# Kernel optimization log

Hardware: AMD Instinct MI355X
Metric: run time of the kernel (lower is better)

## Reference

```python
import jax, jax.numpy as jnp
import numpy as np

N_NODES = 100000
N_EDGES = 1600000
NHID = 128
NFEAT = 256


def setup_inputs() -> dict:
    key = jax.random.key(0)
    ks = jax.random.split(key, 7)
    x = jax.random.normal(ks[0], (N_NODES, NHID), dtype=jnp.float32)
    edge_index = jax.random.randint(ks[1], (2, N_EDGES), 0, N_NODES, dtype=jnp.int64)
    edge_weight = jax.random.uniform(ks[2], (N_EDGES,), dtype=jnp.float32)
    W1 = jax.random.normal(ks[3], (NHID, NHID), dtype=jnp.float32) * (1.0 / np.sqrt(NHID))
    b1 = jnp.zeros((NHID,), dtype=jnp.float32)
    W2 = jax.random.normal(ks[4], (NHID, NFEAT), dtype=jnp.float32) * (1.0 / np.sqrt(NHID))
    b2 = jnp.zeros((NFEAT,), dtype=jnp.float32)
    return {"x": x, "edge_weight": edge_weight, "W1": W1, "b1": b1,
            "W2": W2, "b2": b2, "edge_index": edge_index}


def _gcn_layer(x, W, b, src, dst, w, num_nodes):
    # support = x @ W ; out = spmm(adj, support) + b  (adj given as weighted edge list)
    support = x @ W                                  # [N, d_out]
    msg = support[src] * w[:, None]                  # gather + scale: [E, d_out]
    agg = jax.ops.segment_sum(msg, dst, num_segments=num_nodes)  # scatter-add: [N, d_out]
    return agg + b


def reference(x, edge_weight, W1, b1, W2, b2, edge_index):
    src, dst = edge_index[0], edge_index[1]
    n = x.shape[0]
    # layer 1: GCN -> ReLU (dropout p=0 in eval mode -> identity)
    h = jax.nn.relu(_gcn_layer(x, W1, b1, src, dst, edge_weight, n))
    # layer 2: GCN -> ReLU
    out = jax.nn.relu(_gcn_layer(h, W2, b2, src, dst, edge_weight, n))
    return out
```

## Files before the change

kernel.cpp:

```cpp
#include <hip/hip_runtime.h>
#include <hip/hip_bf16.h>

#define NHID 128
#define NBLK 512
#define FCAP 4096

typedef __attribute__((ext_vector_type(8))) short short8v;
typedef __attribute__((ext_vector_type(4))) float f32x4;

__device__ __forceinline__ unsigned short f32_to_bf16(float f) {
    unsigned u = __float_as_uint(f);
    u += 0x7fffu + ((u >> 16) & 1u);
    return (unsigned short)(u >> 16);
}


__global__ __launch_bounds__(256) void coarse_hist_kernel(const int* __restrict__ dst, int E,
                                                          int nbuck, int per,
                                                          int* __restrict__ ghist) {
    __shared__ int h[1024];
    for (int i = threadIdx.x; i < nbuck; i += 256) h[i] = 0;
    __syncthreads();
    int b0 = blockIdx.x * per;
    int b1 = min(E, b0 + per);
    int e = b0 + threadIdx.x * 4;
    for (; e + 4 <= b1; e += 1024) {
        int4 d4 = *reinterpret_cast<const int4*>(&dst[e]);
        atomicAdd(&h[d4.x >> 7], 1);
        atomicAdd(&h[d4.y >> 7], 1);
        atomicAdd(&h[d4.z >> 7], 1);
        atomicAdd(&h[d4.w >> 7], 1);
    }
    for (; e < b1; ++e) atomicAdd(&h[dst[e] >> 7], 1);
    __syncthreads();
    for (int i = threadIdx.x; i < nbuck; i += 256)
        ghist[(size_t)i * NBLK + blockIdx.x] = h[i];
}

__global__ __launch_bounds__(256) void block_sum_kernel(const int* __restrict__ counts, int n,
                                                        int* __restrict__ bsums) {
    __shared__ int red[256];
    int tid = threadIdx.x;
    int base = blockIdx.x * 2048 + tid * 8;
    int s = 0;
#pragma unroll
    for (int i = 0; i < 8; ++i) {
        int idx = base + i;
        if (idx < n) s += counts[idx];
    }
    red[tid] = s;
    __syncthreads();
    for (int off = 128; off > 0; off >>= 1) {
        if (tid < off) red[tid] += red[tid + off];
        __syncthreads();
    }
    if (tid == 0) bsums[blockIdx.x] = red[0];
}

__global__ __launch_bounds__(256) void scan_bsums_kernel(const int* __restrict__ bsums, int nb,
                                                         int* __restrict__ boffs) {
    __shared__ int ws[4];
    int tid = threadIdx.x;
    int lane = tid & 63;
    int wv = tid >> 6;
    int orig = (tid < nb) ? bsums[tid] : 0;
    int v = orig;
#pragma unroll
    for (int off = 1; off < 64; off <<= 1) {
        int u = __shfl_up(v, off, 64);
        if (lane >= off) v += u;
    }
    if (lane == 63) ws[wv] = v;
    __syncthreads();
    int add = 0;
    for (int w = 0; w < wv; ++w) add += ws[w];
    v += add;
    if (tid < nb) boffs[tid] = v - orig;
    if (tid == nb - 1) boffs[nb] = v;
}

__global__ __launch_bounds__(256) void scan_write_kernel(const int* __restrict__ counts, int n,
                                                         const int* __restrict__ boffs, int nb,
                                                         int* __restrict__ out) {
    __shared__ int wsum[4];
    int tid = threadIdx.x;
    int lane = tid & 63;
    int wv = tid >> 6;
    int base = blockIdx.x * 2048 + tid * 8;

    int v[8];
    int s = 0;
#pragma unroll
    for (int i = 0; i < 8; ++i) {
        int idx = base + i;
        v[i] = (idx < n) ? counts[idx] : 0;
        s += v[i];
    }
    int incl = s;
#pragma unroll
    for (int off = 1; off < 64; off <<= 1) {
        int u = __shfl_up(incl, off, 64);
        if (lane >= off) incl += u;
    }
    if (lane == 63) wsum[wv] = incl;
    __syncthreads();
    int wexcl = 0;
    for (int w = 0; w < wv; ++w) wexcl += wsum[w];

    int run = boffs[blockIdx.x] + wexcl + (incl - s);
#pragma unroll
    for (int i = 0; i < 8; ++i) {
        int idx = base + i;
        if (idx < n) out[idx] = run;
        run += v[i];
    }
    if (blockIdx.x == 0 && tid == 0) out[n] = boffs[nb];
}

__global__ __launch_bounds__(256) void partition_kernel(const int* __restrict__ src,
                                                        const int* __restrict__ dst,
                                                        const float* __restrict__ w, int E,
                                                        int nbuck, int per,
                                                        const int* __restrict__ gofs,
                                                        uint2* __restrict__ coarse) {
    __shared__ int cur[1024];
    for (int i = threadIdx.x; i < nbuck; i += 256)
        cur[i] = gofs[(size_t)i * NBLK + blockIdx.x];
    __syncthreads();
    int b0 = blockIdx.x * per;
    int b1 = min(E, b0 + per);
    int e = b0 + threadIdx.x * 4;
    for (; e + 4 <= b1; e += 1024) {
        int4 d4 = *reinterpret_cast<const int4*>(&dst[e]);
        int4 s4 = *reinterpret_cast<const int4*>(&src[e]);
        float4 w4 = *reinterpret_cast<const float4*>(&w[e]);
        int p0 = atomicAdd(&cur[d4.x >> 7], 1);
        int p1 = atomicAdd(&cur[d4.y >> 7], 1);
        int p2 = atomicAdd(&cur[d4.z >> 7], 1);
        int p3 = atomicAdd(&cur[d4.w >> 7], 1);
        coarse[p0] = make_uint2((unsigned)s4.x | ((unsigned)(d4.x & 127) << 17), __float_as_uint(w4.x));
        coarse[p1] = make_uint2((unsigned)s4.y | ((unsigned)(d4.y & 127) << 17), __float_as_uint(w4.y));
        coarse[p2] = make_uint2((unsigned)s4.z | ((unsigned)(d4.z & 127) << 17), __float_as_uint(w4.z));
        coarse[p3] = make_uint2((unsigned)s4.w | ((unsigned)(d4.w & 127) << 17), __float_as_uint(w4.w));
    }
    for (; e < b1; ++e) {
        int d = dst[e];
        int pos = atomicAdd(&cur[d >> 7], 1);
        coarse[pos] = make_uint2((unsigned)src[e] | ((unsigned)(d & 127) << 17),
                                 __float_as_uint(w[e]));
    }
}

__global__ __launch_bounds__(256) void fine_kernel(const uint2* __restrict__ coarse,
                                                   const int* __restrict__ gofs, int N, int E,
                                                   int* __restrict__ row_ptr,
                                                   int* __restrict__ src_s,
                                                   float* __restrict__ w_s) {
    __shared__ uint2 stash[FCAP];
    __shared__ int hist[128];
    __shared__ int excl[128];
    int b = blockIdx.x;
    int gstart = gofs[(size_t)b * NBLK];
    int gend = gofs[(size_t)(b + 1) * NBLK];
    int cnt = gend - gstart;
    int tid = threadIdx.x;
    if (tid < 128) hist[tid] = 0;
    __syncthreads();
    for (int i = tid; i < cnt; i += 256) {
        uint2 e = coarse[gstart + i];
        if (i < FCAP) stash[i] = e;
        atomicAdd(&hist[(e.x >> 17) & 127], 1);
    }
    __syncthreads();
    if (tid < 64) {
        int a = hist[tid];
        int c = hist[tid + 64];
        int ia = a, ic = c;
#pragma unroll
        for (int off = 1; off < 64; off <<= 1) {
            int u = __shfl_up(ia, off, 64);
            if (tid >= off) ia += u;
            u = __shfl_up(ic, off, 64);
            if (tid >= off) ic += u;
        }
        int totA = __shfl(ia, 63, 64);
        excl[tid] = ia - a;
        excl[tid + 64] = totA + ic - c;
    }
    __syncthreads();
    int node0 = b << 7;
    if (tid < 128 && node0 + tid < N) row_ptr[node0 + tid] = gstart + excl[tid];
    if (b == 0 && tid == 0) row_ptr[N] = E;
    if (tid < 128) hist[tid] = excl[tid];
    __syncthreads();
    for (int i = tid; i < cnt; i += 256) {
        uint2 e = (i < FCAP) ? stash[i] : coarse[gstart + i];
        int dl = (e.x >> 17) & 127;
        int pos = atomicAdd(&hist[dl], 1);
        src_s[gstart + pos] = (int)((e.x & 0x1FFFFu) << 8);
        w_s[gstart + pos] = __uint_as_float(e.y);
    }
}

__global__ void convert_f32_bf16(const float* __restrict__ x, unsigned short* __restrict__ xb,
                                 size_t n4) {
    size_t stride = (size_t)gridDim.x * blockDim.x;
    for (size_t i = (size_t)blockIdx.x * blockDim.x + threadIdx.x; i < n4; i += stride) {
        float4 v = reinterpret_cast<const float4*>(x)[i];
        ushort4 o = make_ushort4(f32_to_bf16(v.x), f32_to_bf16(v.y), f32_to_bf16(v.z),
                                 f32_to_bf16(v.w));
        reinterpret_cast<ushort4*>(xb)[i] = o;
    }
}

__global__ __launch_bounds__(256) void transpose_w_bf16(const float* __restrict__ W,
                                                        unsigned short* __restrict__ WT,
                                                        int K, int N) {
    __shared__ float t[32][33];
    int n0 = blockIdx.x * 32, k0 = blockIdx.y * 32;
    int tx = threadIdx.x & 31;
    int ty = threadIdx.x >> 5;
#pragma unroll
    for (int i = 0; i < 32; i += 8)
        t[ty + i][tx] = W[(size_t)(k0 + ty + i) * N + n0 + tx];
    __syncthreads();
#pragma unroll
    for (int i = 0; i < 32; i += 8)
        WT[(size_t)(n0 + ty + i) * K + k0 + tx] = f32_to_bf16(t[tx][ty + i]);
}

__global__ __launch_bounds__(256) void spmm_csr_bf16(const unsigned short* __restrict__ X,
                                                     const int* __restrict__ src_s,
                                                     const float* __restrict__ w_s,
                                                     const int* __restrict__ row_ptr,
                                                     unsigned short* __restrict__ out, int n) {
    const int lane = threadIdx.x & 63;
    const int grp = lane >> 4;
    const int q = lane & 15;
    const char* Xq = (const char*)X + q * 16;
    const int nwaves = gridDim.x * 4;

    for (int node = blockIdx.x * 4 + (threadIdx.x >> 6); node < n; node += nwaves) {
        int beg = row_ptr[node];
        int end = row_ptr[node + 1];

        float acc[8];
#pragma unroll
        for (int j = 0; j < 8; ++j) acc[j] = 0.f;

        for (int e0 = beg; e0 < end; e0 += 64) {
            int cnt = min(64, end - e0);
            int sb = 0;
            float ww = 0.f;
            if (lane < cnt) {
                sb = src_s[e0 + lane];
                ww = w_s[e0 + lane];
            }
            for (int i = 0; i < cnt; i += 16) {
                unsigned sx[4];
                float wx[4];
#pragma unroll
                for (int u = 0; u < 4; ++u) {
                    sx[u] = (unsigned)__shfl(sb, i + u * 4 + grp, 64);
                    wx[u] = __shfl(ww, i + u * 4 + grp, 64);
                }
                uint4 v[4];
#pragma unroll
                for (int u = 0; u < 4; ++u)
                    v[u] = *reinterpret_cast<const uint4*>(Xq + sx[u]);
#pragma unroll
                for (int u = 0; u < 4; ++u) {
                    unsigned pw;
                    pw = v[u].x;
                    acc[0] += wx[u] * __uint_as_float(pw << 16);
                    acc[1] += wx[u] * __uint_as_float(pw & 0xffff0000u);
                    pw = v[u].y;
                    acc[2] += wx[u] * __uint_as_float(pw << 16);
                    acc[3] += wx[u] * __uint_as_float(pw & 0xffff0000u);
                    pw = v[u].z;
                    acc[4] += wx[u] * __uint_as_float(pw << 16);
                    acc[5] += wx[u] * __uint_as_float(pw & 0xffff0000u);
                    pw = v[u].w;
                    acc[6] += wx[u] * __uint_as_float(pw << 16);
                    acc[7] += wx[u] * __uint_as_float(pw & 0xffff0000u);
                }
            }
        }

#pragma unroll
        for (int j = 0; j < 8; ++j) {
            acc[j] += __shfl_xor(acc[j], 16, 64);
            acc[j] += __shfl_xor(acc[j], 32, 64);
        }

        if (grp == 0) {
            short8v o;
#pragma unroll
            for (int j = 0; j < 8; ++j) o[j] = (short)f32_to_bf16(acc[j]);
            *reinterpret_cast<short8v*>(&out[(size_t)node * NHID + q * 8]) = o;
        }
    }
}

template <int DOUT, bool OUT_BF16>
__global__ __launch_bounds__(256) void gemm_mfma(const unsigned short* __restrict__ Xb,
                                                 const unsigned short* __restrict__ WT,
                                                 const float* __restrict__ bias,
                                                 void* __restrict__ outv, int nrows) {
    __shared__ unsigned short Ab[128 * 128];
    __shared__ unsigned short Bb[128 * 128];
    const int row0 = blockIdx.x * 128;
    const int col0 = blockIdx.y * 128;
    const int tid = threadIdx.x;
    const int lane = tid & 63;
    const int wid = tid >> 6;
    const int waveM = wid >> 1;
    const int waveN = wid & 1;

    {
        const int c = tid & 15;
        int r = tid >> 4;
#pragma unroll
        for (int p = 0; p < 8; ++p, r += 16) {
            int row = row0 + r;
            uint4 va = make_uint4(0, 0, 0, 0);
            if (row < nrows) va = *reinterpret_cast<const uint4*>(&Xb[(size_t)row * 128 + c * 8]);
            uint4 vb = *reinterpret_cast<const uint4*>(&WT[(size_t)(col0 + r) * 128 + c * 8]);
            int cs = (c ^ (r & 15)) * 8;
            *reinterpret_cast<uint4*>(&Ab[r * 128 + cs]) = va;
            *reinterpret_cast<uint4*>(&Bb[r * 128 + cs]) = vb;
        }
    }
    __syncthreads();

    const int lr = lane & 15;
    const int lk = lane >> 4;

    f32x4 acc[4][4];
#pragma unroll
    for (int m = 0; m < 4; ++m)
#pragma unroll
        for (int nn = 0; nn < 4; ++nn) acc[m][nn] = (f32x4){0.f, 0.f, 0.f, 0.f};

#pragma unroll
    for (int ks = 0; ks < 4; ++ks) {
        short8v a[4], b[4];
#pragma unroll
        for (int m = 0; m < 4; ++m) {
            int row = waveM * 64 + m * 16 + lr;
            int c16 = (ks * 4 + lk) ^ (row & 15);
            a[m] = *reinterpret_cast<const short8v*>(&Ab[row * 128 + c16 * 8]);
        }
#pragma unroll
        for (int nn = 0; nn < 4; ++nn) {
            int rowb = waveN * 64 + nn * 16 + lr;
            int c16 = (ks * 4 + lk) ^ (rowb & 15);
            b[nn] = *reinterpret_cast<const short8v*>(&Bb[rowb * 128 + c16 * 8]);
        }
#pragma unroll
        for (int m = 0; m < 4; ++m)
#pragma unroll
            for (int nn = 0; nn < 4; ++nn)
                acc[m][nn] = __builtin_amdgcn_mfma_f32_16x16x32_bf16(a[m], b[nn], acc[m][nn], 0, 0, 0);
    }

    float bj[4];
#pragma unroll
    for (int nn = 0; nn < 4; ++nn) bj[nn] = bias[col0 + waveN * 64 + nn * 16 + lr];

#pragma unroll
    for (int m = 0; m < 4; ++m) {
        int rbase = row0 + waveM * 64 + m * 16 + lk * 4;
#pragma unroll
        for (int reg = 0; reg < 4; ++reg) {
            int r = rbase + reg;
            if (r >= nrows) continue;
#pragma unroll
            for (int nn = 0; nn < 4; ++nn) {
                int cidx = col0 + waveN * 64 + nn * 16 + lr;
                float v = fmaxf(acc[m][nn][reg] + bj[nn], 0.f);
                if (OUT_BF16)
                    ((unsigned short*)outv)[(size_t)r * DOUT + cidx] = f32_to_bf16(v);
                else
                    ((float*)outv)[(size_t)r * DOUT + cidx] = v;
            }
        }
    }
}

extern "C" void kernel_launch(void* const* d_in, const int* in_sizes, int n_in,
                              void* d_out, int out_size, void* d_ws, size_t ws_size,
                              hipStream_t stream) {
    const float* x  = (const float*)d_in[0];
    const float* ew = (const float*)d_in[1];
    const float* W1 = (const float*)d_in[2];
    const float* b1 = (const float*)d_in[3];
    const float* W2 = (const float*)d_in[4];
    const float* b2 = (const float*)d_in[5];
    const int*   ei = (const int*)d_in[6];

    const int N = in_sizes[0] / NHID;
    const int E = in_sizes[1];
    const int* src = ei;
    const int* dst = ei + E;

    const int nbuck = (N + 127) >> 7;
    const int n2 = nbuck * NBLK;
    const int nb2 = (n2 + 2047) / 2048;
    const int per = (((E + NBLK - 1) / NBLK) + 3) & ~3;

    auto align256 = [](size_t v) { return (v + 255) & ~(size_t)255; };
    char* p = (char*)d_ws;
    unsigned short* xb  = (unsigned short*)p; p += align256((size_t)N * NHID * 2);
    unsigned short* gb  = (unsigned short*)p; p += align256((size_t)N * NHID * 2);
    unsigned short* hb  = (unsigned short*)p; p += align256((size_t)N * NHID * 2);
    unsigned short* W1T = (unsigned short*)p; p += align256((size_t)128 * 128 * 2);
    unsigned short* W2T = (unsigned short*)p; p += align256((size_t)256 * 128 * 2);
    int*   ghist   = (int*)p;   p += align256((size_t)(n2 + 1) * 4);
    int*   gofs    = (int*)p;   p += align256((size_t)(n2 + 1) * 4);
    int*   row_ptr = (int*)p;   p += align256((size_t)(N + 1) * 4);
    int*   src_s   = (int*)p;   p += align256((size_t)E * 4);
    float* w_s     = (float*)p; p += align256((size_t)E * 4);
    uint2* coarse  = (uint2*)p; p += align256((size_t)E * 8);
    int*   bsums   = (int*)p;   p += align256((size_t)256 * 4);
    int*   boffs   = (int*)p;   p += align256((size_t)260 * 4);

    coarse_hist_kernel<<<NBLK, 256, 0, stream>>>(dst, E, nbuck, per, ghist);
    block_sum_kernel<<<nb2, 256, 0, stream>>>(ghist, n2, bsums);
    scan_bsums_kernel<<<1, 256, 0, stream>>>(bsums, nb2, boffs);
    scan_write_kernel<<<nb2, 256, 0, stream>>>(ghist, n2, boffs, nb2, gofs);
    partition_kernel<<<NBLK, 256, 0, stream>>>(src, dst, ew, E, nbuck, per, gofs, coarse);
    fine_kernel<<<nbuck, 256, 0, stream>>>(coarse, gofs, N, E, row_ptr, src_s, w_s);

    convert_f32_bf16<<<2048, 256, 0, stream>>>(x, xb, (size_t)N * NHID / 4);
    {
        dim3 g1(128 / 32, 128 / 32);
        transpose_w_bf16<<<g1, 256, 0, stream>>>(W1, W1T, 128, 128);
        dim3 g2(256 / 32, 128 / 32);
        transpose_w_bf16<<<g2, 256, 0, stream>>>(W2, W2T, 128, 256);
    }

    spmm_csr_bf16<<<2048, 256, 0, stream>>>(xb, src_s, w_s, row_ptr, gb, N);
    {
        dim3 grid((N + 127) / 128, 1);
        gemm_mfma<128, true><<<grid, 256, 0, stream>>>(gb, W1T, b1, hb, N);
    }

    spmm_csr_bf16<<<2048, 256, 0, stream>>>(hb, src_s, w_s, row_ptr, gb, N);
    {
        dim3 grid((N + 127) / 128, 2);
        gemm_mfma<256, false><<<grid, 256, 0, stream>>>(gb, W2T, b2, (float*)d_out, N);
    }
}
```

Measured before the change: 252.5 us.

## Interleave src/weight into one edge array and process two nodes per wave in SpMM

The fine sort kernel now writes the source offset and weight as one packed uint2 per edge, so SpMM fetches both with a single 8-byte load instead of two separate arrays. The SpMM kernel now gives each wave a pair of adjacent nodes and runs their edge loops together, issuing gathers for both nodes in the same iteration. This doubles the loads in flight per wave (average degree is about 16) and amortizes row_ptr reads. In exchange it raises register pressure, which can lower occupancy, and a wave waits on the longer of its two rows.

```diff
diff --git a/kernel.cpp b/kernel.cpp
--- a/kernel.cpp
+++ b/kernel.cpp
@@ -154,8 +154,7 @@
 __global__ __launch_bounds__(256) void fine_kernel(const uint2* __restrict__ coarse,
                                                    const int* __restrict__ gofs, int N, int E,
                                                    int* __restrict__ row_ptr,
-                                                   int* __restrict__ src_s,
-                                                   float* __restrict__ w_s) {
+                                                   uint2* __restrict__ edata) {
     __shared__ uint2 stash[FCAP];
     __shared__ int hist[128];
     __shared__ int excl[128];
@@ -197,8 +196,7 @@
         uint2 e = (i < FCAP) ? stash[i] : coarse[gstart + i];
         int dl = (e.x >> 17) & 127;
         int pos = atomicAdd(&hist[dl], 1);
-        src_s[gstart + pos] = (int)((e.x & 0x1FFFFu) << 8);
-        w_s[gstart + pos] = __uint_as_float(e.y);
+        edata[gstart + pos] = make_uint2((e.x & 0x1FFFFu) << 8, e.y);
     }
 }
 
@@ -229,9 +227,25 @@
         WT[(size_t)(n0 + ty + i) * K + k0 + tx] = f32_to_bf16(t[tx][ty + i]);
 }
 
+#define FMA8(acc, wx, v)                                    \
+    do {                                                    \
+        unsigned pw;                                        \
+        pw = (v).x;                                         \
+        acc[0] += (wx) * __uint_as_float(pw << 16);         \
+        acc[1] += (wx) * __uint_as_float(pw & 0xffff0000u); \
+        pw = (v).y;                                         \
+        acc[2] += (wx) * __uint_as_float(pw << 16);         \
+        acc[3] += (wx) * __uint_as_float(pw & 0xffff0000u); \
+        pw = (v).z;                                         \
+        acc[4] += (wx) * __uint_as_float(pw << 16);         \
+        acc[5] += (wx) * __uint_as_float(pw & 0xffff0000u); \
+        pw = (v).w;                                         \
+        acc[6] += (wx) * __uint_as_float(pw << 16);         \
+        acc[7] += (wx) * __uint_as_float(pw & 0xffff0000u); \
+    } while (0)
+
 __global__ __launch_bounds__(256) void spmm_csr_bf16(const unsigned short* __restrict__ X,
-                                                     const int* __restrict__ src_s,
-                                                     const float* __restrict__ w_s,
+                                                     const uint2* __restrict__ edata,
                                                      const int* __restrict__ row_ptr,
                                                      unsigned short* __restrict__ out, int n) {
     const int lane = threadIdx.x & 63;
@@ -239,65 +253,79 @@
     const int q = lane & 15;
     const char* Xq = (const char*)X + q * 16;
     const int nwaves = gridDim.x * 4;
-
-    for (int node = blockIdx.x * 4 + (threadIdx.x >> 6); node < n; node += nwaves) {
-        int beg = row_ptr[node];
-        int end = row_ptr[node + 1];
-
-        float acc[8];
-#pragma unroll
-        for (int j = 0; j < 8; ++j) acc[j] = 0.f;
-
-        for (int e0 = beg; e0 < end; e0 += 64) {
-            int cnt = min(64, end - e0);
-            int sb = 0;
-            float ww = 0.f;
-            if (lane < cnt) {
-                sb = src_s[e0 + lane];
-                ww = w_s[e0 + lane];
+    const int npairs = (n + 1) >> 1;
+
+    for (int pi = blockIdx.x * 4 + (threadIdx.x >> 6); pi < npairs; pi += nwaves) {
+        int nA = pi * 2;
+        int nB = nA + 1;
+        bool hasB = nB < n;
+        int begA = row_ptr[nA];
+        int endA = row_ptr[nA + 1];
+        int begB = endA;
+        int endB = hasB ? row_ptr[nB + 1] : endA;
+
+        float accA[8], accB[8];
+#pragma unroll
+        for (int j = 0; j < 8; ++j) { accA[j] = 0.f; accB[j] = 0.f; }
+
+        int eA = begA, eB = begB;
+        while (eA < endA || eB < endB) {
+            int cntA = endA - eA; cntA = cntA > 64 ? 64 : (cntA < 0 ? 0 : cntA);
+            int cntB = endB - eB; cntB = cntB > 64 ? 64 : (cntB < 0 ? 0 : cntB);
+            unsigned sbA = 0, sbB = 0;
+            float wwA = 0.f, wwB = 0.f;
+            if (lane < cntA) {
+                uint2 ed = edata[eA + lane];
+                sbA = ed.x; wwA = __uint_as_float(ed.y);
             }
-            for (int i = 0; i < cnt; i += 16) {
-                unsigned sx[4];
-                float wx[4];
+            if (lane < cntB) {
+                uint2 ed = edata[eB + lane];
+                sbB = ed.x; wwB = __uint_as_float(ed.y);
+            }
+            int itmax = cntA > cntB ? cntA : cntB;
+            for (int i = 0; i < itmax; i += 16) {
+                unsigned sxA[4], sxB[4];
+                float wxA[4], wxB[4];
 #pragma unroll
                 for (int u = 0; u < 4; ++u) {
-                    sx[u] = (unsigned)__shfl(sb, i + u * 4 + grp, 64);
-                    wx[u] = __shfl(ww, i + u * 4 + grp, 64);
+                    sxA[u] = (unsigned)__shfl((int)sbA, i + u * 4 + grp, 64);
+                    wxA[u] = __shfl(wwA, i + u * 4 + grp, 64);
+                    sxB[u] = (unsigned)__shfl((int)sbB, i + u * 4 + grp, 64);
+                    wxB[u] = __shfl(wwB, i + u * 4 + grp, 64);
                 }
-                uint4 v[4];
-#pragma unroll
-                for (int u = 0; u < 4; ++u)
-                    v[u] = *reinterpret_cast<const uint4*>(Xq + sx[u]);
+                uint4 vA[4], vB[4];
+#pragma unroll
+                for (int u = 0; u < 4; ++u) vA[u] = *reinterpret_cast<const uint4*>(Xq + sxA[u]);
+#pragma unroll
+                for (int u = 0; u < 4; ++u) vB[u] = *reinterpret_cast<const uint4*>(Xq + sxB[u]);
 #pragma unroll
                 for (int u = 0; u < 4; ++u) {
-                    unsigned pw;
-                    pw = v[u].x;
-                    acc[0] += wx[u] * __uint_as_float(pw << 16);
-                    acc[1] += wx[u] * __uint_as_float(pw & 0xffff0000u);
-                    pw = v[u].y;
-                    acc[2] += wx[u] * __uint_as_float(pw << 16);
-                    acc[3] += wx[u] * __uint_as_float(pw & 0xffff0000u);
-                    pw = v[u].z;
-                    acc[4] += wx[u] * __uint_as_float(pw << 16);
-                    acc[5] += wx[u] * __uint_as_float(pw & 0xffff0000u);
-                    pw = v[u].w;
-                    acc[6] += wx[u] * __uint_as_float(pw << 16);
-                    acc[7] += wx[u] * __uint_as_float(pw & 0xffff0000u);
+                    FMA8(accA, wxA[u], vA[u]);
+                    FMA8(accB, wxB[u], vB[u]);
                 }
             }
+            eA += 64;
+            eB += 64;
         }
 
 #pragma unroll
         for (int j = 0; j < 8; ++j) {
-            acc[j] += __shfl_xor(acc[j], 16, 64);
-            acc[j] += __shfl_xor(acc[j], 32, 64);
+            accA[j] += __shfl_xor(accA[j], 16, 64);
+            accA[j] += __shfl_xor(accA[j], 32, 64);
+            accB[j] += __shfl_xor(accB[j], 16, 64);
+            accB[j] += __shfl_xor(accB[j], 32, 64);
         }
 
         if (grp == 0) {
             short8v o;
 #pragma unroll
-            for (int j = 0; j < 8; ++j) o[j] = (short)f32_to_bf16(acc[j]);
-            *reinterpret_cast<short8v*>(&out[(size_t)node * NHID + q * 8]) = o;
+            for (int j = 0; j < 8; ++j) o[j] = (short)f32_to_bf16(accA[j]);
+            *reinterpret_cast<short8v*>(&out[(size_t)nA * NHID + q * 8]) = o;
+        } else if (grp == 1 && hasB) {
+            short8v o;
+#pragma unroll
+            for (int j = 0; j < 8; ++j) o[j] = (short)f32_to_bf16(accB[j]);
+            *reinterpret_cast<short8v*>(&out[(size_t)nB * NHID + q * 8]) = o;
         }
     }
 }
@@ -419,8 +447,7 @@
     int*   ghist   = (int*)p;   p += align256((size_t)(n2 + 1) * 4);
     int*   gofs    = (int*)p;   p += align256((size_t)(n2 + 1) * 4);
     int*   row_ptr = (int*)p;   p += align256((size_t)(N + 1) * 4);
-    int*   src_s   = (int*)p;   p += align256((size_t)E * 4);
-    float* w_s     = (float*)p; p += align256((size_t)E * 4);
+    uint2* edata   = (uint2*)p; p += align256((size_t)E * 8);
     uint2* coarse  = (uint2*)p; p += align256((size_t)E * 8);
     int*   bsums   = (int*)p;   p += align256((size_t)256 * 4);
     int*   boffs   = (int*)p;   p += align256((size_t)260 * 4);
@@ -430,7 +457,7 @@
     scan_bsums_kernel<<<1, 256, 0, stream>>>(bsums, nb2, boffs);
     scan_write_kernel<<<nb2, 256, 0, stream>>>(ghist, n2, boffs, nb2, gofs);
     partition_kernel<<<NBLK, 256, 0, stream>>>(src, dst, ew, E, nbuck, per, gofs, coarse);
-    fine_kernel<<<nbuck, 256, 0, stream>>>(coarse, gofs, N, E, row_ptr, src_s, w_s);
+    fine_kernel<<<nbuck, 256, 0, stream>>>(coarse, gofs, N, E, row_ptr, edata);
 
     convert_f32_bf16<<<2048, 256, 0, stream>>>(x, xb, (size_t)N * NHID / 4);
     {
@@ -440,13 +467,13 @@
         transpose_w_bf16<<<g2, 256, 0, stream>>>(W2, W2T, 128, 256);
     }
 
-    spmm_csr_bf16<<<2048, 256, 0, stream>>>(xb, src_s, w_s, row_ptr, gb, N);
+    spmm_csr_bf16<<<2048, 256, 0, stream>>>(xb, edata, row_ptr, gb, N);
     {
         dim3 grid((N + 127) / 128, 1);
         gemm_mfma<128, true><<<grid, 256, 0, stream>>>(gb, W1T, b1, hb, N);
     }
 
-    spmm_csr_bf16<<<2048, 256, 0, stream>>>(hb, src_s, w_s, row_ptr, gb, N);
+    spmm_csr_bf16<<<2048, 256, 0, stream>>>(hb, edata, row_ptr, gb, N);
     {
         dim3 grid((N + 127) / 128, 2);
         gemm_mfma<256, false><<<grid, 256, 0, stream>>>(gb, W2T, b2, (float*)d_out, N);
```

Measured after the change: 278.2 us. +10.2%, slower.

## Store features in 16-column slabs and pack edge src+weight into one word

Applied to the files above, without the earlier changes.

Feature matrices are now stored as 8 column slabs of 16 bf16 values per node. The SpMM grid is split so each group of 256 blocks handles one slab, which keeps each slab's working set (about 3.2 MB) cache-resident during the random gathers. Edge source index and weight are packed into a single 32-bit word (17-bit index, 15-bit truncated bf16-like weight), halving edge-list traffic. The GEMM load and store paths are changed to match the slab layout. The trade-off is lower weight precision and 8x more passes over the edge list.

```diff
diff --git a/kernel.cpp b/kernel.cpp
--- a/kernel.cpp
+++ b/kernel.cpp
@@ -154,8 +154,7 @@
 __global__ __launch_bounds__(256) void fine_kernel(const uint2* __restrict__ coarse,
                                                    const int* __restrict__ gofs, int N, int E,
                                                    int* __restrict__ row_ptr,
-                                                   int* __restrict__ src_s,
-                                                   float* __restrict__ w_s) {
+                                                   unsigned* __restrict__ edata) {
     __shared__ uint2 stash[FCAP];
     __shared__ int hist[128];
     __shared__ int excl[128];
@@ -197,19 +196,32 @@
         uint2 e = (i < FCAP) ? stash[i] : coarse[gstart + i];
         int dl = (e.x >> 17) & 127;
         int pos = atomicAdd(&hist[dl], 1);
-        src_s[gstart + pos] = (int)((e.x & 0x1FFFFu) << 8);
-        w_s[gstart + pos] = __uint_as_float(e.y);
-    }
-}
-
-__global__ void convert_f32_bf16(const float* __restrict__ x, unsigned short* __restrict__ xb,
-                                 size_t n4) {
-    size_t stride = (size_t)gridDim.x * blockDim.x;
-    for (size_t i = (size_t)blockIdx.x * blockDim.x + threadIdx.x; i < n4; i += stride) {
-        float4 v = reinterpret_cast<const float4*>(x)[i];
-        ushort4 o = make_ushort4(f32_to_bf16(v.x), f32_to_bf16(v.y), f32_to_bf16(v.z),
-                                 f32_to_bf16(v.w));
-        reinterpret_cast<ushort4*>(xb)[i] = o;
+        unsigned u = e.y;
+        unsigned w15 = ((u + 0x7fffu + ((u >> 16) & 1u)) >> 16) & 0x7FFFu;
+        edata[gstart + pos] = (w15 << 17) | (e.x & 0x1FFFFu);
+    }
+}
+
+__global__ void convert_x_slab(const float* __restrict__ x, unsigned short* __restrict__ xb,
+                               int n) {
+    int total = n * 8;
+    int stride = gridDim.x * blockDim.x;
+    for (int t = blockIdx.x * blockDim.x + threadIdx.x; t < total; t += stride) {
+        int node = t >> 3, sl = t & 7;
+        const float4* src = reinterpret_cast<const float4*>(x + (size_t)node * 128 + sl * 16);
+        float4 f0 = src[0], f1 = src[1], f2 = src[2], f3 = src[3];
+        uint4 o0, o1;
+        o0.x = (unsigned)f32_to_bf16(f0.x) | ((unsigned)f32_to_bf16(f0.y) << 16);
+        o0.y = (unsigned)f32_to_bf16(f0.z) | ((unsigned)f32_to_bf16(f0.w) << 16);
+        o0.z = (unsigned)f32_to_bf16(f1.x) | ((unsigned)f32_to_bf16(f1.y) << 16);
+        o0.w = (unsigned)f32_to_bf16(f1.z) | ((unsigned)f32_to_bf16(f1.w) << 16);
+        o1.x = (unsigned)f32_to_bf16(f2.x) | ((unsigned)f32_to_bf16(f2.y) << 16);
+        o1.y = (unsigned)f32_to_bf16(f2.z) | ((unsigned)f32_to_bf16(f2.w) << 16);
+        o1.z = (unsigned)f32_to_bf16(f3.x) | ((unsigned)f32_to_bf16(f3.y) << 16);
+        o1.w = (unsigned)f32_to_bf16(f3.z) | ((unsigned)f32_to_bf16(f3.w) << 16);
+        unsigned short* dst = xb + (size_t)sl * n * 16 + (size_t)node * 16;
+        reinterpret_cast<uint4*>(dst)[0] = o0;
+        reinterpret_cast<uint4*>(dst)[1] = o1;
     }
 }
 
@@ -229,75 +241,50 @@
         WT[(size_t)(n0 + ty + i) * K + k0 + tx] = f32_to_bf16(t[tx][ty + i]);
 }
 
-__global__ __launch_bounds__(256) void spmm_csr_bf16(const unsigned short* __restrict__ X,
-                                                     const int* __restrict__ src_s,
-                                                     const float* __restrict__ w_s,
-                                                     const int* __restrict__ row_ptr,
-                                                     unsigned short* __restrict__ out, int n) {
+__global__ __launch_bounds__(256) void spmm_slab_bf16(const unsigned short* __restrict__ Xslab,
+                                                      const unsigned* __restrict__ edata,
+                                                      const int* __restrict__ row_ptr,
+                                                      unsigned short* __restrict__ outSlab,
+                                                      int n) {
     const int lane = threadIdx.x & 63;
-    const int grp = lane >> 4;
-    const int q = lane & 15;
-    const char* Xq = (const char*)X + q * 16;
-    const int nwaves = gridDim.x * 4;
-
-    for (int node = blockIdx.x * 4 + (threadIdx.x >> 6); node < n; node += nwaves) {
+    const int esub = lane >> 2;
+    const int cq = lane & 3;
+    const int slice = blockIdx.x >> 8;
+    const char* Xb = (const char*)(Xslab + (size_t)slice * n * 16) + cq * 8;
+    unsigned short* slabO = outSlab + (size_t)slice * n * 16;
+    const int wstart = ((blockIdx.x & 255) << 2) + (threadIdx.x >> 6);
+
+    for (int node = wstart; node < n; node += 1024) {
         int beg = row_ptr[node];
         int end = row_ptr[node + 1];
-
-        float acc[8];
-#pragma unroll
-        for (int j = 0; j < 8; ++j) acc[j] = 0.f;
-
+        float a0 = 0.f, a1 = 0.f, a2 = 0.f, a3 = 0.f;
         for (int e0 = beg; e0 < end; e0 += 64) {
             int cnt = min(64, end - e0);
-            int sb = 0;
-            float ww = 0.f;
-            if (lane < cnt) {
-                sb = src_s[e0 + lane];
-                ww = w_s[e0 + lane];
+            unsigned m = 0;
+            if (lane < cnt) m = __builtin_nontemporal_load(&edata[e0 + lane]);
+            for (int i = 0; i < cnt; i += 16) {
+                unsigned mm = (unsigned)__shfl((int)m, i + esub, 64);
+                float w = __uint_as_float((mm & 0xFFFE0000u) >> 1);
+                unsigned off = (mm & 0x1FFFFu) << 5;
+                uint2 v = *reinterpret_cast<const uint2*>(Xb + off);
+                a0 += w * __uint_as_float(v.x << 16);
+                a1 += w * __uint_as_float(v.x & 0xffff0000u);
+                a2 += w * __uint_as_float(v.y << 16);
+                a3 += w * __uint_as_float(v.y & 0xffff0000u);
             }
-            for (int i = 0; i < cnt; i += 16) {
-                unsigned sx[4];
-                float wx[4];
-#pragma unroll
-                for (int u = 0; u < 4; ++u) {
-                    sx[u] = (unsigned)__shfl(sb, i + u * 4 + grp, 64);
-                    wx[u] = __shfl(ww, i + u * 4 + grp, 64);
-                }
-                uint4 v[4];
-#pragma unroll
-                for (int u = 0; u < 4; ++u)
-                    v[u] = *reinterpret_cast<const uint4*>(Xq + sx[u]);
-#pragma unroll
-                for (int u = 0; u < 4; ++u) {
-                    unsigned pw;
-                    pw = v[u].x;
-                    acc[0] += wx[u] * __uint_as_float(pw << 16);
-                    acc[1] += wx[u] * __uint_as_float(pw & 0xffff0000u);
-                    pw = v[u].y;
-                    acc[2] += wx[u] * __uint_as_float(pw << 16);
-                    acc[3] += wx[u] * __uint_as_float(pw & 0xffff0000u);
-                    pw = v[u].z;
-                    acc[4] += wx[u] * __uint_as_float(pw << 16);
-                    acc[5] += wx[u] * __uint_as_float(pw & 0xffff0000u);
-                    pw = v[u].w;
-                    acc[6] += wx[u] * __uint_as_float(pw << 16);
-                    acc[7] += wx[u] * __uint_as_float(pw & 0xffff0000u);
-                }
-            }
-        }
-
-#pragma unroll
-        for (int j = 0; j < 8; ++j) {
-            acc[j] += __shfl_xor(acc[j], 16, 64);
-            acc[j] += __shfl_xor(acc[j], 32, 64);
-        }
-
-        if (grp == 0) {
-            short8v o;
-#pragma unroll
-            for (int j = 0; j < 8; ++j) o[j] = (short)f32_to_bf16(acc[j]);
-            *reinterpret_cast<short8v*>(&out[(size_t)node * NHID + q * 8]) = o;
+        }
+#pragma unroll
+        for (int d = 4; d < 64; d <<= 1) {
+            a0 += __shfl_xor(a0, d, 64);
+            a1 += __shfl_xor(a1, d, 64);
+            a2 += __shfl_xor(a2, d, 64);
+            a3 += __shfl_xor(a3, d, 64);
+        }
+        if (lane < 4) {
+            uint2 o;
+            o.x = (unsigned)f32_to_bf16(a0) | ((unsigned)f32_to_bf16(a1) << 16);
+            o.y = (unsigned)f32_to_bf16(a2) | ((unsigned)f32_to_bf16(a3) << 16);
+            *reinterpret_cast<uint2*>(slabO + (size_t)node * 16 + lane * 4) = o;
         }
     }
 }
@@ -320,11 +307,14 @@
     {
         const int c = tid & 15;
         int r = tid >> 4;
+        const size_t slabStride = (size_t)nrows * 16;
 #pragma unroll
         for (int p = 0; p < 8; ++p, r += 16) {
             int row = row0 + r;
             uint4 va = make_uint4(0, 0, 0, 0);
-            if (row < nrows) va = *reinterpret_cast<const uint4*>(&Xb[(size_t)row * 128 + c * 8]);
+            if (row < nrows)
+                va = *reinterpret_cast<const uint4*>(Xb + (size_t)(c >> 1) * slabStride +
+                                                     (size_t)row * 16 + (c & 1) * 8);
             uint4 vb = *reinterpret_cast<const uint4*>(&WT[(size_t)(col0 + r) * 128 + c * 8]);
             int cs = (c ^ (r & 15)) * 8;
             *reinterpret_cast<uint4*>(&Ab[r * 128 + cs]) = va;
@@ -379,10 +369,13 @@
             for (int nn = 0; nn < 4; ++nn) {
                 int cidx = col0 + waveN * 64 + nn * 16 + lr;
                 float v = fmaxf(acc[m][nn][reg] + bj[nn], 0.f);
-                if (OUT_BF16)
-                    ((unsigned short*)outv)[(size_t)r * DOUT + cidx] = f32_to_bf16(v);
-                else
+                if (OUT_BF16) {
+                    unsigned short* ob = (unsigned short*)outv;
+                    ob[(size_t)(cidx >> 4) * nrows * 16 + (size_t)r * 16 + (cidx & 15)] =
+                        f32_to_bf16(v);
+                } else {
                     ((float*)outv)[(size_t)r * DOUT + cidx] = v;
+                }
             }
         }
     }
@@ -416,23 +409,22 @@
     unsigned short* hb  = (unsigned short*)p; p += align256((size_t)N * NHID * 2);
     unsigned short* W1T = (unsigned short*)p; p += align256((size_t)128 * 128 * 2);
     unsigned short* W2T = (unsigned short*)p; p += align256((size_t)256 * 128 * 2);
-    int*   ghist   = (int*)p;   p += align256((size_t)(n2 + 1) * 4);
-    int*   gofs    = (int*)p;   p += align256((size_t)(n2 + 1) * 4);
-    int*   row_ptr = (int*)p;   p += align256((size_t)(N + 1) * 4);
-    int*   src_s   = (int*)p;   p += align256((size_t)E * 4);
-    float* w_s     = (float*)p; p += align256((size_t)E * 4);
-    uint2* coarse  = (uint2*)p; p += align256((size_t)E * 8);
-    int*   bsums   = (int*)p;   p += align256((size_t)256 * 4);
-    int*   boffs   = (int*)p;   p += align256((size_t)260 * 4);
+    int*   ghist   = (int*)p;      p += align256((size_t)(n2 + 1) * 4);
+    int*   gofs    = (int*)p;      p += align256((size_t)(n2 + 1) * 4);
+    int*   row_ptr = (int*)p;      p += align256((size_t)(N + 1) * 4);
+    unsigned* edata = (unsigned*)p; p += align256((size_t)E * 4);
+    uint2* coarse  = (uint2*)p;    p += align256((size_t)E * 8);
+    int*   bsums   = (int*)p;      p += align256((size_t)256 * 4);
+    int*   boffs   = (int*)p;      p += align256((size_t)260 * 4);
 
     coarse_hist_kernel<<<NBLK, 256, 0, stream>>>(dst, E, nbuck, per, ghist);
     block_sum_kernel<<<nb2, 256, 0, stream>>>(ghist, n2, bsums);
     scan_bsums_kernel<<<1, 256, 0, stream>>>(bsums, nb2, boffs);
     scan_write_kernel<<<nb2, 256, 0, stream>>>(ghist, n2, boffs, nb2, gofs);
     partition_kernel<<<NBLK, 256, 0, stream>>>(src, dst, ew, E, nbuck, per, gofs, coarse);
-    fine_kernel<<<nbuck, 256, 0, stream>>>(coarse, gofs, N, E, row_ptr, src_s, w_s);
-
-    convert_f32_bf16<<<2048, 256, 0, stream>>>(x, xb, (size_t)N * NHID / 4);
+    fine_kernel<<<nbuck, 256, 0, stream>>>(coarse, gofs, N, E, row_ptr, edata);
+
+    convert_x_slab<<<2048, 256, 0, stream>>>(x, xb, N);
     {
         dim3 g1(128 / 32, 128 / 32);
         transpose_w_bf16<<<g1, 256, 0, stream>>>(W1, W1T, 128, 128);
@@ -440,13 +432,13 @@
         transpose_w_bf16<<<g2, 256, 0, stream>>>(W2, W2T, 128, 256);
     }
 
-    spmm_csr_bf16<<<2048, 256, 0, stream>>>(xb, src_s, w_s, row_ptr, gb, N);
+    spmm_slab_bf16<<<2048, 256, 0, stream>>>(xb, edata, row_ptr, gb, N);
     {
         dim3 grid((N + 127) / 128, 1);
         gemm_mfma<128, true><<<grid, 256, 0, stream>>>(gb, W1T, b1, hb, N);
     }
 
-    spmm_csr_bf16<<<2048, 256, 0, stream>>>(hb, src_s, w_s, row_ptr, gb, N);
+    spmm_slab_bf16<<<2048, 256, 0, stream>>>(hb, edata, row_ptr, gb, N);
     {
         dim3 grid((N + 127) / 128, 2);
         gemm_mfma<256, false><<<grid, 256, 0, stream>>>(gb, W2T, b2, (float*)d_out, N);
```

After: 564.3 us. +123.5%, slower.

## Pack edge src/weight into 64-bit records and software-pipeline SpMM gathers

Applied to the files above, without the earlier changes.

The sorted edge source offsets and weights are interleaved into a single 64-bit array, so each edge is one load instead of two from separate arrays. The SpMM kernel now assigns exactly one node per wave, launching one wave per node instead of a grid-stride loop. It double-buffers 16-edge steps so the feature gathers for later steps are issued while earlier ones are being accumulated, with metadata read through nontemporal loads. The final fp32 output store also becomes nontemporal. The pipeline adds register pressure, and its prefetch reads past the row end return zeros, which the lane and end guards handle.

```diff
diff --git a/kernel.cpp b/kernel.cpp
--- a/kernel.cpp
+++ b/kernel.cpp
@@ -154,8 +154,7 @@
 __global__ __launch_bounds__(256) void fine_kernel(const uint2* __restrict__ coarse,
                                                    const int* __restrict__ gofs, int N, int E,
                                                    int* __restrict__ row_ptr,
-                                                   int* __restrict__ src_s,
-                                                   float* __restrict__ w_s) {
+                                                   unsigned long long* __restrict__ edata) {
     __shared__ uint2 stash[FCAP];
     __shared__ int hist[128];
     __shared__ int excl[128];
@@ -197,8 +196,8 @@
         uint2 e = (i < FCAP) ? stash[i] : coarse[gstart + i];
         int dl = (e.x >> 17) & 127;
         int pos = atomicAdd(&hist[dl], 1);
-        src_s[gstart + pos] = (int)((e.x & 0x1FFFFu) << 8);
-        w_s[gstart + pos] = __uint_as_float(e.y);
+        unsigned long long off = (unsigned long long)((e.x & 0x1FFFFu) << 8);
+        edata[gstart + pos] = off | ((unsigned long long)e.y << 32);
     }
 }
 
@@ -229,77 +228,100 @@
         WT[(size_t)(n0 + ty + i) * K + k0 + tx] = f32_to_bf16(t[tx][ty + i]);
 }
 
+#define FMA8(acc, wx, v)                                    \
+    do {                                                    \
+        unsigned pw;                                        \
+        pw = (v).x;                                         \
+        acc[0] += (wx) * __uint_as_float(pw << 16);         \
+        acc[1] += (wx) * __uint_as_float(pw & 0xffff0000u); \
+        pw = (v).y;                                         \
+        acc[2] += (wx) * __uint_as_float(pw << 16);         \
+        acc[3] += (wx) * __uint_as_float(pw & 0xffff0000u); \
+        pw = (v).z;                                         \
+        acc[4] += (wx) * __uint_as_float(pw << 16);         \
+        acc[5] += (wx) * __uint_as_float(pw & 0xffff0000u); \
+        pw = (v).w;                                         \
+        acc[6] += (wx) * __uint_as_float(pw << 16);         \
+        acc[7] += (wx) * __uint_as_float(pw & 0xffff0000u); \
+    } while (0)
+
 __global__ __launch_bounds__(256) void spmm_csr_bf16(const unsigned short* __restrict__ X,
-                                                     const int* __restrict__ src_s,
-                                                     const float* __restrict__ w_s,
+                                                     const unsigned long long* __restrict__ edata,
                                                      const int* __restrict__ row_ptr,
                                                      unsigned short* __restrict__ out, int n) {
     const int lane = threadIdx.x & 63;
     const int grp = lane >> 4;
     const int q = lane & 15;
     const char* Xq = (const char*)X + q * 16;
-    const int nwaves = gridDim.x * 4;
-
-    for (int node = blockIdx.x * 4 + (threadIdx.x >> 6); node < n; node += nwaves) {
-        int beg = row_ptr[node];
-        int end = row_ptr[node + 1];
-
-        float acc[8];
-#pragma unroll
-        for (int j = 0; j < 8; ++j) acc[j] = 0.f;
-
-        for (int e0 = beg; e0 < end; e0 += 64) {
-            int cnt = min(64, end - e0);
-            int sb = 0;
-            float ww = 0.f;
-            if (lane < cnt) {
-                sb = src_s[e0 + lane];
-                ww = w_s[e0 + lane];
-            }
-            for (int i = 0; i < cnt; i += 16) {
-                unsigned sx[4];
-                float wx[4];
-#pragma unroll
-                for (int u = 0; u < 4; ++u) {
-                    sx[u] = (unsigned)__shfl(sb, i + u * 4 + grp, 64);
-                    wx[u] = __shfl(ww, i + u * 4 + grp, 64);
-                }
-                uint4 v[4];
-#pragma unroll
-                for (int u = 0; u < 4; ++u)
-                    v[u] = *reinterpret_cast<const uint4*>(Xq + sx[u]);
-#pragma unroll
-                for (int u = 0; u < 4; ++u) {
-                    unsigned pw;
-                    pw = v[u].x;
-                    acc[0] += wx[u] * __uint_as_float(pw << 16);
-                    acc[1] += wx[u] * __uint_as_float(pw & 0xffff0000u);
-                    pw = v[u].y;
-                    acc[2] += wx[u] * __uint_as_float(pw << 16);
-                    acc[3] += wx[u] * __uint_as_float(pw & 0xffff0000u);
-                    pw = v[u].z;
-                    acc[4] += wx[u] * __uint_as_float(pw << 16);
-                    acc[5] += wx[u] * __uint_as_float(pw & 0xffff0000u);
-                    pw = v[u].w;
-                    acc[6] += wx[u] * __uint_as_float(pw << 16);
-                    acc[7] += wx[u] * __uint_as_float(pw & 0xffff0000u);
-                }
-            }
-        }
-
-#pragma unroll
-        for (int j = 0; j < 8; ++j) {
-            acc[j] += __shfl_xor(acc[j], 16, 64);
-            acc[j] += __shfl_xor(acc[j], 32, 64);
-        }
-
-        if (grp == 0) {
-            short8v o;
-#pragma unroll
-            for (int j = 0; j < 8; ++j) o[j] = (short)f32_to_bf16(acc[j]);
-            *reinterpret_cast<short8v*>(&out[(size_t)node * NHID + q * 8]) = o;
-        }
-    }
+
+    int node = blockIdx.x * 4 + (threadIdx.x >> 6);
+    if (node >= n) return;
+    int beg = row_ptr[node];
+    int end = row_ptr[node + 1];
+    int nsteps = (end - beg + 15) >> 4;
+
+    float acc[8];
+#pragma unroll
+    for (int j = 0; j < 8; ++j) acc[j] = 0.f;
+
+#define LM(s, md)                                                                     \
+    do {                                                                              \
+        int idx_ = beg + ((s) << 4) + lane;                                           \
+        md = (lane < 16 && idx_ < end) ? __builtin_nontemporal_load(&edata[idx_])     \
+                                       : 0ULL;                                        \
+    } while (0)
+
+#define ISSUE(md, v, w)                                                         \
+    do {                                                                        \
+        unsigned mlo_ = (unsigned)(md);                                         \
+        unsigned mhi_ = (unsigned)((md) >> 32);                                 \
+        _Pragma("unroll") for (int u_ = 0; u_ < 4; ++u_) {                      \
+            unsigned off_ = (unsigned)__shfl((int)mlo_, u_ * 4 + grp, 64);      \
+            w[u_] = __uint_as_float((unsigned)__shfl((int)mhi_, u_ * 4 + grp, 64)); \
+            v[u_] = *reinterpret_cast<const uint4*>(Xq + off_);                 \
+        }                                                                       \
+    } while (0)
+
+#define FMA4(v, w)                                            \
+    do {                                                      \
+        _Pragma("unroll") for (int u_ = 0; u_ < 4; ++u_) {    \
+            FMA8(acc, w[u_], v[u_]);                          \
+        }                                                     \
+    } while (0)
+
+    unsigned long long mA, mB;
+    uint4 vA[4], vB[4];
+    float wA[4], wB[4];
+    LM(0, mA);
+    LM(1, mB);
+    ISSUE(mA, vA, wA);
+    ISSUE(mB, vB, wB);
+    LM(2, mA);
+    LM(3, mB);
+    for (int s = 0; s < nsteps; s += 2) {
+        FMA4(vA, wA);
+        ISSUE(mA, vA, wA);
+        LM(s + 4, mA);
+        FMA4(vB, wB);
+        ISSUE(mB, vB, wB);
+        LM(s + 5, mB);
+    }
+
+#pragma unroll
+    for (int j = 0; j < 8; ++j) {
+        acc[j] += __shfl_xor(acc[j], 16, 64);
+        acc[j] += __shfl_xor(acc[j], 32, 64);
+    }
+
+    if (grp == 0) {
+        short8v o;
+#pragma unroll
+        for (int j = 0; j < 8; ++j) o[j] = (short)f32_to_bf16(acc[j]);
+        *reinterpret_cast<short8v*>(&out[(size_t)node * NHID + q * 8]) = o;
+    }
+#undef LM
+#undef ISSUE
+#undef FMA4
 }
 
 template <int DOUT, bool OUT_BF16>
@@ -382,7 +404,7 @@
                 if (OUT_BF16)
                     ((unsigned short*)outv)[(size_t)r * DOUT + cidx] = f32_to_bf16(v);
                 else
-                    ((float*)outv)[(size_t)r * DOUT + cidx] = v;
+                    __builtin_nontemporal_store(v, &((float*)outv)[(size_t)r * DOUT + cidx]);
             }
         }
     }
@@ -419,8 +441,7 @@
     int*   ghist   = (int*)p;   p += align256((size_t)(n2 + 1) * 4);
     int*   gofs    = (int*)p;   p += align256((size_t)(n2 + 1) * 4);
     int*   row_ptr = (int*)p;   p += align256((size_t)(N + 1) * 4);
-    int*   src_s   = (int*)p;   p += align256((size_t)E * 4);
-    float* w_s     = (float*)p; p += align256((size_t)E * 4);
+    unsigned long long* edata = (unsigned long long*)p; p += align256((size_t)E * 8);
     uint2* coarse  = (uint2*)p; p += align256((size_t)E * 8);
     int*   bsums   = (int*)p;   p += align256((size_t)256 * 4);
     int*   boffs   = (int*)p;   p += align256((size_t)260 * 4);
@@ -430,7 +451,7 @@
     scan_bsums_kernel<<<1, 256, 0, stream>>>(bsums, nb2, boffs);
     scan_write_kernel<<<nb2, 256, 0, stream>>>(ghist, n2, boffs, nb2, gofs);
     partition_kernel<<<NBLK, 256, 0, stream>>>(src, dst, ew, E, nbuck, per, gofs, coarse);
-    fine_kernel<<<nbuck, 256, 0, stream>>>(coarse, gofs, N, E, row_ptr, src_s, w_s);
+    fine_kernel<<<nbuck, 256, 0, stream>>>(coarse, gofs, N, E, row_ptr, edata);
 
     convert_f32_bf16<<<2048, 256, 0, stream>>>(x, xb, (size_t)N * NHID / 4);
     {
@@ -440,13 +461,13 @@
         transpose_w_bf16<<<g2, 256, 0, stream>>>(W2, W2T, 128, 256);
     }
 
-    spmm_csr_bf16<<<2048, 256, 0, stream>>>(xb, src_s, w_s, row_ptr, gb, N);
+    spmm_csr_bf16<<<(N + 3) / 4, 256, 0, stream>>>(xb, edata, row_ptr, gb, N);
     {
         dim3 grid((N + 127) / 128, 1);
         gemm_mfma<128, true><<<grid, 256, 0, stream>>>(gb, W1T, b1, hb, N);
     }
 
-    spmm_csr_bf16<<<2048, 256, 0, stream>>>(hb, src_s, w_s, row_ptr, gb, N);
+    spmm_csr_bf16<<<(N + 3) / 4, 256, 0, stream>>>(hb, edata, row_ptr, gb, N);
     {
         dim3 grid((N + 127) / 128, 2);
         gemm_mfma<256, false><<<grid, 256, 0, stream>>>(gb, W2T, b2, (float*)d_out, N);
```

Result: slower. 286.9 us (+13.6%).
